# Optimization experiments

Hardware: AMD Instinct MI355X
Metric: run time of the kernel (lower is better)

Reference implementation:

```python
import jax, jax.numpy as jnp
import numpy as np

GAMMA = 0.3
LOSS_WEIGHT = 1.0
LG2 = 0.6931471805599453
NEG = -1e30  # finite stand-in for -inf to keep grads NaN-free

N, C = 1048576, 32


def setup_inputs() -> dict:
    key = jax.random.key(0)
    k1, k2 = jax.random.split(key)
    cls_score = jax.random.normal(k1, (N, C), dtype=jnp.float32)
    label = jax.random.randint(k2, (N,), 0, C, dtype=jnp.int64)
    return {"cls_score": cls_score, "label": label}


def reference(cls_score, label):
    # log_probs: [N, C]
    log_probs = jax.nn.log_softmax(cls_score, axis=1)
    num_classes = cls_score.shape[1]

    # per-class ground-truth counts ngt_c = sum(label == c)
    counts = jnp.zeros((num_classes,), dtype=log_probs.dtype).at[label].add(1.0)
    present = counts > 0

    # ni_c = logsumexp over points with label==c of log_probs[:, c]
    onehot = label[:, None] == jnp.arange(num_classes)[None, :]  # [N, C] bool
    masked = jnp.where(onehot, log_probs, NEG)
    ni = jax.nn.logsumexp(masked, axis=0)          # [C]

    # npr_c = logsumexp over all points of log_probs[:, c]
    npr = jax.nn.logsumexp(log_probs, axis=0)      # [C]

    log_ngt = jnp.log(jnp.maximum(counts, 1.0))
    log_dice = LG2 + ni - jnp.logaddexp(log_ngt, npr)  # [C], <= 0 for present classes

    neg_log_dice = jnp.where(present, -log_dice, 1.0)  # safe value for absent classes
    losses = jnp.where(present, jnp.power(neg_log_dice, GAMMA), 0.0)

    n_present = present.sum().astype(losses.dtype)
    return LOSS_WEIGHT * losses.sum() / n_present
```

## Files before the change

### kernel.cpp

```cpp
#include <hip/hip_runtime.h>
#include <math.h>


#define P1_BLOCKS 2048
#define P1_THREADS 256

__global__ __launch_bounds__(P1_THREADS) void eld_pass1(
    const float* __restrict__ score, const int* __restrict__ label,
    float4* __restrict__ pack,
    int nrows, int ngroups)
{
    const int tid   = threadIdx.x;
    const int q     = tid & 7;
    const int rslot = tid >> 3;
    const int cbase = q << 2;

    float a_npr0 = 0.f, a_npr1 = 0.f, a_npr2 = 0.f, a_npr3 = 0.f;
    float a_ni0  = 0.f, a_ni1  = 0.f, a_ni2  = 0.f, a_ni3  = 0.f;
    float a_c0   = 0.f, a_c1   = 0.f, a_c2   = 0.f, a_c3   = 0.f;

    for (int g = blockIdx.x; g < ngroups; g += gridDim.x) {
        const int row = g * 32 + rslot;
        if (row < nrows) {
            const float4 v = reinterpret_cast<const float4*>(score)[row * 8 + q];
            float m = fmaxf(fmaxf(v.x, v.y), fmaxf(v.z, v.w));
            m = fmaxf(m, __shfl_xor(m, 1));
            m = fmaxf(m, __shfl_xor(m, 2));
            m = fmaxf(m, __shfl_xor(m, 4));
            const float e0 = __expf(v.x - m);
            const float e1 = __expf(v.y - m);
            const float e2 = __expf(v.z - m);
            const float e3 = __expf(v.w - m);
            float s = (e0 + e1) + (e2 + e3);
            s += __shfl_xor(s, 1);
            s += __shfl_xor(s, 2);
            s += __shfl_xor(s, 4);
            const float inv = __builtin_amdgcn_rcpf(s);
            const float p0 = e0 * inv, p1 = e1 * inv, p2 = e2 * inv, p3 = e3 * inv;
            a_npr0 += p0; a_npr1 += p1; a_npr2 += p2; a_npr3 += p3;
            const int lab = label[row];
            if (lab == cbase + 0) { a_ni0 += p0; a_c0 += 1.f; }
            if (lab == cbase + 1) { a_ni1 += p1; a_c1 += 1.f; }
            if (lab == cbase + 2) { a_ni2 += p2; a_c2 += 1.f; }
            if (lab == cbase + 3) { a_ni3 += p3; a_c3 += 1.f; }
        }
    }

#pragma unroll
    for (int off = 8; off < 64; off <<= 1) {
        a_npr0 += __shfl_xor(a_npr0, off);
        a_npr1 += __shfl_xor(a_npr1, off);
        a_npr2 += __shfl_xor(a_npr2, off);
        a_npr3 += __shfl_xor(a_npr3, off);
        a_ni0  += __shfl_xor(a_ni0,  off);
        a_ni1  += __shfl_xor(a_ni1,  off);
        a_ni2  += __shfl_xor(a_ni2,  off);
        a_ni3  += __shfl_xor(a_ni3,  off);
        a_c0   += __shfl_xor(a_c0,   off);
        a_c1   += __shfl_xor(a_c1,   off);
        a_c2   += __shfl_xor(a_c2,   off);
        a_c3   += __shfl_xor(a_c3,   off);
    }

    __shared__ float lds[3][4][32];
    const int wave = tid >> 6;
    const int lane = tid & 63;
    if (lane < 8) {
        lds[0][wave][lane * 4 + 0] = a_npr0;
        lds[0][wave][lane * 4 + 1] = a_npr1;
        lds[0][wave][lane * 4 + 2] = a_npr2;
        lds[0][wave][lane * 4 + 3] = a_npr3;
        lds[1][wave][lane * 4 + 0] = a_ni0;
        lds[1][wave][lane * 4 + 1] = a_ni1;
        lds[1][wave][lane * 4 + 2] = a_ni2;
        lds[1][wave][lane * 4 + 3] = a_ni3;
        lds[2][wave][lane * 4 + 0] = a_c0;
        lds[2][wave][lane * 4 + 1] = a_c1;
        lds[2][wave][lane * 4 + 2] = a_c2;
        lds[2][wave][lane * 4 + 3] = a_c3;
    }
    __syncthreads();
    if (tid < 32) {
        float n = 0.f, i2 = 0.f, k = 0.f;
#pragma unroll
        for (int w = 0; w < 4; ++w) {
            n  += lds[0][w][tid];
            i2 += lds[1][w][tid];
            k  += lds[2][w][tid];
        }
        pack[blockIdx.x * 32 + tid] = make_float4(n, i2, k, 0.f);
    }
}

__global__ __launch_bounds__(1024) void eld_pass2(
    const float4* __restrict__ pack, float* __restrict__ out, int nblk)
{
    __shared__ float4 l_acc[32][32];
    __shared__ float l_loss[32], l_pres[32];
    const int tid = threadIdx.x;
    const int c = tid & 31;
    const int s = tid >> 5;
    float n = 0.f, i2 = 0.f, k = 0.f;
#pragma unroll 16
    for (int b = s; b < nblk; b += 32) {
        const float4 v = pack[b * 32 + c];
        n += v.x; i2 += v.y; k += v.z;
    }
    l_acc[s][c] = make_float4(n, i2, k, 0.f);
    __syncthreads();
    if (tid < 32) {
        float N_ = 0.f, I = 0.f, K = 0.f;
#pragma unroll
        for (int w = 0; w < 32; ++w) {
            const float4 v = l_acc[w][tid];
            N_ += v.x; I += v.y; K += v.z;
        }
        float loss = 0.f, pres = 0.f;
        if (K > 0.f) {
            float nld = logf((K + N_) / (2.f * I));
            nld = fmaxf(nld, 0.f);
            loss = powf(nld, 0.3f);
            pres = 1.f;
        }
        l_loss[tid] = loss;
        l_pres[tid] = pres;
    }
    __syncthreads();
    if (tid == 0) {
        float sum = 0.f, np = 0.f;
#pragma unroll
        for (int c2 = 0; c2 < 32; ++c2) { sum += l_loss[c2]; np += l_pres[c2]; }
        out[0] = sum / np;
    }
}

extern "C" void kernel_launch(void* const* d_in, const int* in_sizes, int n_in,
                              void* d_out, int out_size, void* d_ws, size_t ws_size,
                              hipStream_t stream) {
    const float* score = (const float*)d_in[0];
    const int*   label = (const int*)d_in[1];
    float* out = (float*)d_out;

    const int nrows = in_sizes[0] / 32;
    const int ngroups = (nrows + 31) / 32;

    int nblk = P1_BLOCKS;
    if (nblk > ngroups) nblk = ngroups;

    float4* pack = (float4*)d_ws;

    eld_pass1<<<nblk, P1_THREADS, 0, stream>>>(score, label, pack, nrows, ngroups);
    eld_pass2<<<1, 1024, 0, stream>>>(pack, out, nblk);
}
```

Measured before the change: 40.76 us.

## Split final reduction across 32 per-class blocks with transposed partial layout

Pass 1 now writes its per-block partial sums in class-major (structure-of-arrays) order instead of as interleaved float4 records. Pass 2 becomes 32 blocks, one per class, each reducing contiguous partials with wave shuffles, and a new third kernel combines the per-class losses. The goal is to spread the second-stage reduction over many compute units instead of running it in one 1024-thread block. The cost is an extra kernel launch and scattered strided stores at the end of pass 1.

Result: faster. 35.92 us (-11.9%).

```diff
diff --git a/kernel.cpp b/kernel.cpp
--- a/kernel.cpp
+++ b/kernel.cpp
@@ -2,13 +2,13 @@
 #include <math.h>
 
 
-#define P1_BLOCKS 2048
-#define P1_THREADS 256
+#define NBLK1 2048
+#define NTHR1 256
 
-__global__ __launch_bounds__(P1_THREADS) void eld_pass1(
+__global__ __launch_bounds__(NTHR1) void eld_pass1(
     const float* __restrict__ score, const int* __restrict__ label,
-    float4* __restrict__ pack,
-    int nrows, int ngroups)
+    float* __restrict__ part,
+    int nrows, int ngroups, int nblk)
 {
     const int tid   = threadIdx.x;
     const int q     = tid & 7;
@@ -88,33 +88,39 @@
             i2 += lds[1][w][tid];
             k  += lds[2][w][tid];
         }
-        pack[blockIdx.x * 32 + tid] = make_float4(n, i2, k, 0.f);
+        part[(size_t)tid * nblk + blockIdx.x]        = n;
+        part[(size_t)(32 + tid) * nblk + blockIdx.x] = i2;
+        part[(size_t)(64 + tid) * nblk + blockIdx.x] = k;
     }
 }
 
-__global__ __launch_bounds__(1024) void eld_pass2(
-    const float4* __restrict__ pack, float* __restrict__ out, int nblk)
+__global__ __launch_bounds__(256) void eld_pass2(
+    const float* __restrict__ part, float* __restrict__ tiny, int nblk)
 {
-    __shared__ float4 l_acc[32][32];
-    __shared__ float l_loss[32], l_pres[32];
+    const int c = blockIdx.x;
     const int tid = threadIdx.x;
-    const int c = tid & 31;
-    const int s = tid >> 5;
+    const float* npr = part + (size_t)c * nblk;
+    const float* ni  = part + (size_t)(32 + c) * nblk;
+    const float* cnt = part + (size_t)(64 + c) * nblk;
+
     float n = 0.f, i2 = 0.f, k = 0.f;
-#pragma unroll 16
-    for (int b = s; b < nblk; b += 32) {
-        const float4 v = pack[b * 32 + c];
-        n += v.x; i2 += v.y; k += v.z;
+    for (int b = tid; b < nblk; b += 256) {
+        n += npr[b]; i2 += ni[b]; k += cnt[b];
     }
-    l_acc[s][c] = make_float4(n, i2, k, 0.f);
+#pragma unroll
+    for (int off = 1; off < 64; off <<= 1) {
+        n  += __shfl_xor(n, off);
+        i2 += __shfl_xor(i2, off);
+        k  += __shfl_xor(k, off);
+    }
+    __shared__ float ln[4], li[4], lk[4];
+    const int wave = tid >> 6;
+    if ((tid & 63) == 0) { ln[wave] = n; li[wave] = i2; lk[wave] = k; }
     __syncthreads();
-    if (tid < 32) {
-        float N_ = 0.f, I = 0.f, K = 0.f;
-#pragma unroll
-        for (int w = 0; w < 32; ++w) {
-            const float4 v = l_acc[w][tid];
-            N_ += v.x; I += v.y; K += v.z;
-        }
+    if (tid == 0) {
+        float N_ = ln[0] + ln[1] + ln[2] + ln[3];
+        float I  = li[0] + li[1] + li[2] + li[3];
+        float K  = lk[0] + lk[1] + lk[2] + lk[3];
         float loss = 0.f, pres = 0.f;
         if (K > 0.f) {
             float nld = logf((K + N_) / (2.f * I));
@@ -122,16 +128,23 @@
             loss = powf(nld, 0.3f);
             pres = 1.f;
         }
-        l_loss[tid] = loss;
-        l_pres[tid] = pres;
+        tiny[c]      = loss;
+        tiny[32 + c] = pres;
     }
-    __syncthreads();
-    if (tid == 0) {
-        float sum = 0.f, np = 0.f;
+}
+
+__global__ __launch_bounds__(64) void eld_pass3(
+    const float* __restrict__ tiny, float* __restrict__ out)
+{
+    const int lane = threadIdx.x;
+    float l = (lane < 32) ? tiny[lane]      : 0.f;
+    float p = (lane < 32) ? tiny[32 + lane] : 0.f;
 #pragma unroll
-        for (int c2 = 0; c2 < 32; ++c2) { sum += l_loss[c2]; np += l_pres[c2]; }
-        out[0] = sum / np;
+    for (int off = 1; off < 64; off <<= 1) {
+        l += __shfl_xor(l, off);
+        p += __shfl_xor(p, off);
     }
+    if (lane == 0) out[0] = l / p;
 }
 
 extern "C" void kernel_launch(void* const* d_in, const int* in_sizes, int n_in,
@@ -144,11 +157,13 @@
     const int nrows = in_sizes[0] / 32;
     const int ngroups = (nrows + 31) / 32;
 
-    int nblk = P1_BLOCKS;
+    int nblk = NBLK1;
     if (nblk > ngroups) nblk = ngroups;
 
-    float4* pack = (float4*)d_ws;
+    float* part = (float*)d_ws;
+    float* tiny = part + (size_t)96 * nblk;
 
-    eld_pass1<<<nblk, P1_THREADS, 0, stream>>>(score, label, pack, nrows, ngroups);
-    eld_pass2<<<1, 1024, 0, stream>>>(pack, out, nblk);
+    eld_pass1<<<nblk, NTHR1, 0, stream>>>(score, label, part, nrows, ngroups, nblk);
+    eld_pass2<<<32, 256, 0, stream>>>(part, tiny, nblk);
+    eld_pass3<<<1, 64, 0, stream>>>(tiny, out);
 }
```
